# Kernel tuning notes

Hardware: AMD Instinct MI355X
Metric: run time of the kernel (lower is better)

## Reference

```python
import jax, jax.numpy as jnp
import numpy as np

N, M, D, NNZ, H = 1024, 1024, 128, 32768, 256


def setup_inputs() -> dict:
    key = jax.random.key(0)
    k_x, k_v, k_e, k_w1, k_b1, k_w2, k_b2 = jax.random.split(key, 7)
    X = jax.random.normal(k_x, (N, D), dtype=jnp.float32)
    V = jax.random.randint(k_v, (NNZ,), 0, N)
    E = jax.random.randint(k_e, (NNZ,), 0, M)
    # nn.Linear(2D, 256) and nn.Linear(256, 1) params (Kaiming-uniform-ish init)
    lim1 = 1.0 / np.sqrt(2 * D)
    W1 = jax.random.uniform(k_w1, (2 * D, H), minval=-lim1, maxval=lim1, dtype=jnp.float32)
    b1 = jax.random.uniform(k_b1, (H,), minval=-lim1, maxval=lim1, dtype=jnp.float32)
    lim2 = 1.0 / np.sqrt(H)
    W2 = jax.random.uniform(k_w2, (H, 1), minval=-lim2, maxval=lim2, dtype=jnp.float32)
    b2 = jax.random.uniform(k_b2, (1,), minval=-lim2, maxval=lim2, dtype=jnp.float32)
    return {"X": X, "V": V, "E": E, "W1": W1, "b1": b1, "W2": W2, "b2": b2}


def reference(X, V, E, W1, b1, W2, b2):
    # scatter-mean: eX[m] = mean of X[V[j]] over j with E[j] == m  -> [M, D]
    gathered = X[V]  # [NNZ, D]
    sums = jax.ops.segment_sum(gathered, E, num_segments=M)           # [M, D]
    counts = jax.ops.segment_sum(jnp.ones((NNZ,), X.dtype), E, num_segments=M)
    eX = sums / jnp.maximum(counts, 1.0)[:, None]
    # cat([X_broadcast, eX_broadcast], -1) @ W1 == X @ W1[:D] + eX @ W1[D:]
    # avoids materializing the [N, M, 2D] concat; math is identical.
    hx = X @ W1[:D]    # [N, H]
    he = eX @ W1[D:]   # [M, H]
    h = jax.nn.relu(hx[:, None, :] + he[None, :, :] + b1)  # [N, M, H]
    logits = jnp.squeeze(h @ W2, axis=-1) + b2              # [N, M]
    return jax.nn.sigmoid(logits)
```

## Files before the change

### kernel.cpp

```cpp
#include <hip/hip_runtime.h>

#define N_ 1024
#define M_ 1024
#define D_ 128
#define NNZ_ 32768
#define H_ 256

typedef _Float16 h2 __attribute__((ext_vector_type(2)));

__global__ __launch_bounds__(256) void gemm_kernel(
        const float* __restrict__ X, const int* __restrict__ V,
        const int* __restrict__ E, const float* __restrict__ W1,
        const float* __restrict__ b1,
        _Float16* __restrict__ hx, _Float16* __restrict__ heb) {
    __shared__ float sA[16][128];
    __shared__ int s_bkt[8][128];
    __shared__ int s_cnt[8];
    const int t = threadIdx.x;
    const int b = blockIdx.x;

    if (b < 64) {
        const int row0 = b * 16;
        {
            const float4* A4 = (const float4*)(X + row0 * D_);
            float4* S4 = (float4*)&sA[0][0];
            S4[t] = A4[t];
            S4[t + 256] = A4[t + 256];
        }
        __syncthreads();

        float acc[16];
#pragma unroll
        for (int r = 0; r < 16; ++r) acc[r] = 0.f;

        for (int d = 0; d < D_; d += 4) {
            float w0 = W1[(d + 0) * H_ + t];
            float w1 = W1[(d + 1) * H_ + t];
            float w2 = W1[(d + 2) * H_ + t];
            float w3 = W1[(d + 3) * H_ + t];
#pragma unroll
            for (int r = 0; r < 16; ++r) {
                float4 a = *(const float4*)&sA[r][d];
                acc[r] = fmaf(a.x, w0, acc[r]);
                acc[r] = fmaf(a.y, w1, acc[r]);
                acc[r] = fmaf(a.z, w2, acc[r]);
                acc[r] = fmaf(a.w, w3, acc[r]);
            }
        }
#pragma unroll
        for (int r = 0; r < 16; ++r)
            hx[(row0 + r) * H_ + t] = (_Float16)acc[r];
    } else {
        const int m0 = (b - 64) * 8;

        if (t < 8) s_cnt[t] = 0;
        __syncthreads();

        {
            const int4* E4 = (const int4*)E;
            const int4* V4 = (const int4*)V;
#pragma unroll 4
            for (int it = 0; it < NNZ_ / 4 / 256; ++it) {
                int idx = it * 256 + t;
                int4 e4 = E4[idx];
                int4 v4 = V4[idx];
                unsigned r;
                r = (unsigned)(e4.x - m0);
                if (r < 8u) { int s = atomicAdd(&s_cnt[r], 1); s_bkt[r][s & 127] = v4.x; }
                r = (unsigned)(e4.y - m0);
                if (r < 8u) { int s = atomicAdd(&s_cnt[r], 1); s_bkt[r][s & 127] = v4.y; }
                r = (unsigned)(e4.z - m0);
                if (r < 8u) { int s = atomicAdd(&s_cnt[r], 1); s_bkt[r][s & 127] = v4.z; }
                r = (unsigned)(e4.w - m0);
                if (r < 8u) { int s = atomicAdd(&s_cnt[r], 1); s_bkt[r][s & 127] = v4.w; }
            }
        }
        __syncthreads();

        const int d = t & 127;
        const int half = t >> 7;
#pragma unroll
        for (int p = 0; p < 4; ++p) {
            const int r = p * 2 + half;
            const int cnt = min(s_cnt[r], 128);
            float s = 0.f;
            int i = 0;
            for (; i + 4 <= cnt; i += 4) {
                int v0 = s_bkt[r][i], v1 = s_bkt[r][i + 1];
                int v2 = s_bkt[r][i + 2], v3 = s_bkt[r][i + 3];
                s += X[v0 * D_ + d];
                s += X[v1 * D_ + d];
                s += X[v2 * D_ + d];
                s += X[v3 * D_ + d];
            }
            for (; i < cnt; ++i) s += X[s_bkt[r][i] * D_ + d];
            sA[r][d] = s;
        }
        __syncthreads();

        float acc[8];
#pragma unroll
        for (int r = 0; r < 8; ++r) acc[r] = 0.f;

        const float* __restrict__ W = W1 + D_ * H_;
        for (int dd = 0; dd < D_; dd += 4) {
            float w0 = W[(dd + 0) * H_ + t];
            float w1 = W[(dd + 1) * H_ + t];
            float w2 = W[(dd + 2) * H_ + t];
            float w3 = W[(dd + 3) * H_ + t];
#pragma unroll
            for (int r = 0; r < 8; ++r) {
                float4 a = *(const float4*)&sA[r][dd];
                acc[r] = fmaf(a.x, w0, acc[r]);
                acc[r] = fmaf(a.y, w1, acc[r]);
                acc[r] = fmaf(a.z, w2, acc[r]);
                acc[r] = fmaf(a.w, w3, acc[r]);
            }
        }

        const float bias = b1[t];
#pragma unroll
        for (int r = 0; r < 8; ++r) {
            float inv = 1.0f / fmaxf((float)s_cnt[r], 1.0f);
            heb[(m0 + r) * H_ + t] = (_Float16)(acc[r] * inv + bias);
        }
    }
}

__global__ __launch_bounds__(512) void big_kernel(
        const _Float16* __restrict__ hx, const _Float16* __restrict__ heb,
        const float* __restrict__ W2, const float* __restrict__ b2,
        float* __restrict__ out) {
    __shared__ _Float16 sA[64][264];
    __shared__ _Float16 sB[64][264];
    __shared__ h2 sW[H_ / 2];

    const int tid = threadIdx.x;
    const int tx = tid & 15;
    const int ty = tid >> 4;
    const int n0 = blockIdx.y * 64;
    const int m0 = blockIdx.x * 64;

    if (tid < H_ / 2) {
        h2 w;
        w.x = (_Float16)W2[2 * tid];
        w.y = (_Float16)W2[2 * tid + 1];
        sW[tid] = w;
    }

    {
        const float4* A4 = (const float4*)hx;
        const float4* B4 = (const float4*)heb;
#pragma unroll
        for (int it = 0; it < 4; ++it) {
            int lin = it * 512 + tid;
            int row = lin >> 5;
            int c = lin & 31;
            *(float4*)&sA[row][c * 8] = A4[(n0 + row) * 32 + c];
            *(float4*)&sB[row][c * 8] = B4[(m0 + row) * 32 + c];
        }
    }
    __syncthreads();

    float acc[2][4];
#pragma unroll
    for (int i = 0; i < 2; ++i)
#pragma unroll
        for (int j = 0; j < 4; ++j) acc[i][j] = 0.f;

    union Vn { float4 f4; h2 h[4]; };
    const h2 z = {(_Float16)0.f, (_Float16)0.f};

#pragma unroll 4
    for (int hp = 0; hp < H_ / 2; hp += 4) {
        Vn av[2], bv[4], wv;
        wv.f4 = *(const float4*)&sW[hp];
#pragma unroll
        for (int i = 0; i < 2; ++i) av[i].f4 = *(const float4*)&sA[ty + 32 * i][hp * 2];
#pragma unroll
        for (int j = 0; j < 4; ++j) bv[j].f4 = *(const float4*)&sB[tx + 16 * j][hp * 2];
#pragma unroll
        for (int k = 0; k < 4; ++k) {
#pragma unroll
            for (int i = 0; i < 2; ++i) {
#pragma unroll
                for (int j = 0; j < 4; ++j) {
                    h2 t = av[i].h[k] + bv[j].h[k];
                    t = __builtin_elementwise_max(t, z);
                    acc[i][j] = __builtin_amdgcn_fdot2(t, wv.h[k], acc[i][j], false);
                }
            }
        }
    }

    const float bb = b2[0];
#pragma unroll
    for (int i = 0; i < 2; ++i) {
#pragma unroll
        for (int j = 0; j < 4; ++j) {
            float x = acc[i][j] + bb;
            out[(n0 + ty + 32 * i) * M_ + (m0 + tx + 16 * j)] =
                1.0f / (1.0f + __expf(-x));
        }
    }
}

extern "C" void kernel_launch(void* const* d_in, const int* in_sizes, int n_in,
                              void* d_out, int out_size, void* d_ws, size_t ws_size,
                              hipStream_t stream) {
    const float* X  = (const float*)d_in[0];
    const int*   V  = (const int*)d_in[1];
    const int*   E  = (const int*)d_in[2];
    const float* W1 = (const float*)d_in[3];
    const float* b1 = (const float*)d_in[4];
    const float* W2 = (const float*)d_in[5];
    const float* b2 = (const float*)d_in[6];
    float* out = (float*)d_out;

    char* ws = (char*)d_ws;
    _Float16* hx  = (_Float16*)(ws);
    _Float16* heb = (_Float16*)(ws + 524288);

    gemm_kernel<<<192, 256, 0, stream>>>(X, V, E, W1, b1, hx, heb);

    dim3 bgrid(M_ / 64, N_ / 64);
    big_kernel<<<bgrid, 512, 0, stream>>>(hx, heb, W2, b2, out);
}
```

Measured before the change: 113.6 us.

## Unify gemm blocks to handle 4 X rows and 4 segments each

The first kernel's blocks are restructured so every block computes 4 rows of hx and 4 segments of heb, replacing the split of 64 hx blocks and 128 segment blocks with 256 uniform blocks. The E scan now loads V only when one of the four E values falls in the block's range. The aim is to balance the work across blocks, fill more CUs, and cut V loads. In exchange every block scans all of E, so total E traffic grows, and the hx GEMM work per block is smaller, with less reuse of each W1 load.

```diff
diff --git a/kernel.cpp b/kernel.cpp
--- a/kernel.cpp
+++ b/kernel.cpp
@@ -13,74 +13,47 @@
         const int* __restrict__ E, const float* __restrict__ W1,
         const float* __restrict__ b1,
         _Float16* __restrict__ hx, _Float16* __restrict__ heb) {
-    __shared__ float sA[16][128];
-    __shared__ int s_bkt[8][128];
-    __shared__ int s_cnt[8];
+    __shared__ float sA[8][128];
+    __shared__ int s_bkt[4][128];
+    __shared__ int s_cnt[4];
     const int t = threadIdx.x;
     const int b = blockIdx.x;
-
-    if (b < 64) {
-        const int row0 = b * 16;
-        {
-            const float4* A4 = (const float4*)(X + row0 * D_);
-            float4* S4 = (float4*)&sA[0][0];
-            S4[t] = A4[t];
-            S4[t + 256] = A4[t + 256];
-        }
-        __syncthreads();
-
-        float acc[16];
-#pragma unroll
-        for (int r = 0; r < 16; ++r) acc[r] = 0.f;
-
-        for (int d = 0; d < D_; d += 4) {
-            float w0 = W1[(d + 0) * H_ + t];
-            float w1 = W1[(d + 1) * H_ + t];
-            float w2 = W1[(d + 2) * H_ + t];
-            float w3 = W1[(d + 3) * H_ + t];
-#pragma unroll
-            for (int r = 0; r < 16; ++r) {
-                float4 a = *(const float4*)&sA[r][d];
-                acc[r] = fmaf(a.x, w0, acc[r]);
-                acc[r] = fmaf(a.y, w1, acc[r]);
-                acc[r] = fmaf(a.z, w2, acc[r]);
-                acc[r] = fmaf(a.w, w3, acc[r]);
+    const int row0 = b * 4;
+    const int m0 = b * 4;
+
+    if (t < 4) s_cnt[t] = 0;
+    if (t < 128) {
+        ((float4*)&sA[0][0])[t] = ((const float4*)(X + row0 * D_))[t];
+    }
+    __syncthreads();
+
+    {
+        const int4* E4 = (const int4*)E;
+        const int4* V4 = (const int4*)V;
+#pragma unroll 4
+        for (int it = 0; it < NNZ_ / 4 / 256; ++it) {
+            int idx = it * 256 + t;
+            int4 e4 = E4[idx];
+            unsigned r0 = (unsigned)(e4.x - m0);
+            unsigned r1 = (unsigned)(e4.y - m0);
+            unsigned r2 = (unsigned)(e4.z - m0);
+            unsigned r3 = (unsigned)(e4.w - m0);
+            if ((r0 < 4u) | (r1 < 4u) | (r2 < 4u) | (r3 < 4u)) {
+                int4 v4 = V4[idx];
+                if (r0 < 4u) { int s = atomicAdd(&s_cnt[r0], 1); s_bkt[r0][s & 127] = v4.x; }
+                if (r1 < 4u) { int s = atomicAdd(&s_cnt[r1], 1); s_bkt[r1][s & 127] = v4.y; }
+                if (r2 < 4u) { int s = atomicAdd(&s_cnt[r2], 1); s_bkt[r2][s & 127] = v4.z; }
+                if (r3 < 4u) { int s = atomicAdd(&s_cnt[r3], 1); s_bkt[r3][s & 127] = v4.w; }
             }
         }
-#pragma unroll
-        for (int r = 0; r < 16; ++r)
-            hx[(row0 + r) * H_ + t] = (_Float16)acc[r];
-    } else {
-        const int m0 = (b - 64) * 8;
-
-        if (t < 8) s_cnt[t] = 0;
-        __syncthreads();
-
-        {
-            const int4* E4 = (const int4*)E;
-            const int4* V4 = (const int4*)V;
-#pragma unroll 4
-            for (int it = 0; it < NNZ_ / 4 / 256; ++it) {
-                int idx = it * 256 + t;
-                int4 e4 = E4[idx];
-                int4 v4 = V4[idx];
-                unsigned r;
-                r = (unsigned)(e4.x - m0);
-                if (r < 8u) { int s = atomicAdd(&s_cnt[r], 1); s_bkt[r][s & 127] = v4.x; }
-                r = (unsigned)(e4.y - m0);
-                if (r < 8u) { int s = atomicAdd(&s_cnt[r], 1); s_bkt[r][s & 127] = v4.y; }
-                r = (unsigned)(e4.z - m0);
-                if (r < 8u) { int s = atomicAdd(&s_cnt[r], 1); s_bkt[r][s & 127] = v4.z; }
-                r = (unsigned)(e4.w - m0);
-                if (r < 8u) { int s = atomicAdd(&s_cnt[r], 1); s_bkt[r][s & 127] = v4.w; }
-            }
-        }
-        __syncthreads();
-
+    }
+    __syncthreads();
+
+    {
         const int d = t & 127;
         const int half = t >> 7;
 #pragma unroll
-        for (int p = 0; p < 4; ++p) {
+        for (int p = 0; p < 2; ++p) {
             const int r = p * 2 + half;
             const int cnt = min(s_cnt[r], 128);
             float s = 0.f;
@@ -94,36 +67,53 @@
                 s += X[v3 * D_ + d];
             }
             for (; i < cnt; ++i) s += X[s_bkt[r][i] * D_ + d];
-            sA[r][d] = s;
-        }
-        __syncthreads();
-
-        float acc[8];
-#pragma unroll
-        for (int r = 0; r < 8; ++r) acc[r] = 0.f;
-
-        const float* __restrict__ W = W1 + D_ * H_;
-        for (int dd = 0; dd < D_; dd += 4) {
-            float w0 = W[(dd + 0) * H_ + t];
-            float w1 = W[(dd + 1) * H_ + t];
-            float w2 = W[(dd + 2) * H_ + t];
-            float w3 = W[(dd + 3) * H_ + t];
-#pragma unroll
-            for (int r = 0; r < 8; ++r) {
-                float4 a = *(const float4*)&sA[r][dd];
-                acc[r] = fmaf(a.x, w0, acc[r]);
-                acc[r] = fmaf(a.y, w1, acc[r]);
-                acc[r] = fmaf(a.z, w2, acc[r]);
-                acc[r] = fmaf(a.w, w3, acc[r]);
-            }
-        }
-
-        const float bias = b1[t];
-#pragma unroll
-        for (int r = 0; r < 8; ++r) {
-            float inv = 1.0f / fmaxf((float)s_cnt[r], 1.0f);
-            heb[(m0 + r) * H_ + t] = (_Float16)(acc[r] * inv + bias);
-        }
+            sA[4 + r][d] = s;
+        }
+    }
+    __syncthreads();
+
+    float acc[8];
+#pragma unroll
+    for (int r = 0; r < 8; ++r) acc[r] = 0.f;
+
+    const float* __restrict__ Wa = W1;
+    const float* __restrict__ Wb = W1 + D_ * H_;
+    for (int dd = 0; dd < D_; dd += 4) {
+        float wa0 = Wa[(dd + 0) * H_ + t];
+        float wa1 = Wa[(dd + 1) * H_ + t];
+        float wa2 = Wa[(dd + 2) * H_ + t];
+        float wa3 = Wa[(dd + 3) * H_ + t];
+        float wb0 = Wb[(dd + 0) * H_ + t];
+        float wb1 = Wb[(dd + 1) * H_ + t];
+        float wb2 = Wb[(dd + 2) * H_ + t];
+        float wb3 = Wb[(dd + 3) * H_ + t];
+#pragma unroll
+        for (int r = 0; r < 4; ++r) {
+            float4 a = *(const float4*)&sA[r][dd];
+            acc[r] = fmaf(a.x, wa0, acc[r]);
+            acc[r] = fmaf(a.y, wa1, acc[r]);
+            acc[r] = fmaf(a.z, wa2, acc[r]);
+            acc[r] = fmaf(a.w, wa3, acc[r]);
+        }
+#pragma unroll
+        for (int r = 0; r < 4; ++r) {
+            float4 a = *(const float4*)&sA[4 + r][dd];
+            acc[4 + r] = fmaf(a.x, wb0, acc[4 + r]);
+            acc[4 + r] = fmaf(a.y, wb1, acc[4 + r]);
+            acc[4 + r] = fmaf(a.z, wb2, acc[4 + r]);
+            acc[4 + r] = fmaf(a.w, wb3, acc[4 + r]);
+        }
+    }
+
+#pragma unroll
+    for (int r = 0; r < 4; ++r)
+        hx[(row0 + r) * H_ + t] = (_Float16)acc[r];
+
+    const float bias = b1[t];
+#pragma unroll
+    for (int r = 0; r < 4; ++r) {
+        float inv = 1.0f / fmaxf((float)s_cnt[r], 1.0f);
+        heb[(m0 + r) * H_ + t] = (_Float16)(acc[4 + r] * inv + bias);
     }
 }
 
@@ -221,7 +211,7 @@
     _Float16* hx  = (_Float16*)(ws);
     _Float16* heb = (_Float16*)(ws + 524288);
 
-    gemm_kernel<<<192, 256, 0, stream>>>(X, V, E, W1, b1, hx, heb);
+    gemm_kernel<<<256, 256, 0, stream>>>(X, V, E, W1, b1, hx, heb);
 
     dim3 bgrid(M_ / 64, N_ / 64);
     big_kernel<<<bgrid, 512, 0, stream>>>(hx, heb, W2, b2, out);
```

Result: faster. 107.5 us (-5.3%).
